# Optimization experiments

Hardware: AMD Instinct MI355X
Metric: run time of the kernel (lower is better)

## Reference

```python
import jax, jax.numpy as jnp
import numpy as np

N_NODES = 100000
N_EDGES = 1250000
IN_DIM = 64
HID_DIM = 64
EDGE_DIM = 10
BN_EPS = 1e-5


def setup_inputs() -> dict:
    key = jax.random.key(0)
    ks = jax.random.split(key, 10)
    x = jax.random.normal(ks[0], (N_NODES, IN_DIM), dtype=jnp.float32)
    edge_index = jax.random.randint(ks[1], (2, N_EDGES), 0, N_NODES, dtype=jnp.int64)
    edge_attr = jax.random.normal(ks[2], (N_EDGES, EDGE_DIM), dtype=jnp.float32)
    # GINEConv edge projection Linear(edge_dim=10 -> indim)
    W_edge = jax.random.normal(ks[3], (EDGE_DIM, IN_DIM), dtype=jnp.float32) * (1.0 / np.sqrt(EDGE_DIM))
    b_edge = jnp.zeros((IN_DIM,), dtype=jnp.float32)
    # MLP: Linear(indim, hiddendim) -> ReLU -> Linear(hiddendim, hiddendim)
    W1 = jax.random.normal(ks[4], (IN_DIM, HID_DIM), dtype=jnp.float32) * (1.0 / np.sqrt(IN_DIM))
    b1 = jnp.zeros((HID_DIM,), dtype=jnp.float32)
    W2 = jax.random.normal(ks[5], (HID_DIM, HID_DIM), dtype=jnp.float32) * (1.0 / np.sqrt(HID_DIM))
    b2 = jnp.zeros((HID_DIM,), dtype=jnp.float32)
    # BatchNorm1d affine params
    bn_gamma = jnp.ones((HID_DIM,), dtype=jnp.float32)
    bn_beta = jnp.zeros((HID_DIM,), dtype=jnp.float32)
    return {"x": x, "edge_index": edge_index, "edge_attr": edge_attr,
            "W_edge": W_edge, "b_edge": b_edge, "W1": W1, "b1": b1,
            "W2": W2, "b2": b2, "bn_gamma": bn_gamma, "bn_beta": bn_beta}


def reference(x, edge_index, edge_attr, W_edge, b_edge, W1, b1, W2, b2, bn_gamma, bn_beta):
    src, dst = edge_index[0], edge_index[1]
    # message: ReLU(x_j + lin(edge_attr))  [E, indim]
    msg = jax.nn.relu(x[src] + edge_attr @ W_edge + b_edge)
    # sum-aggregate into destination nodes  [N, indim]
    aggr = jax.ops.segment_sum(msg, dst, num_segments=N_NODES)
    # GIN update: nn((1+eps)*x + aggr), eps=0
    h = x + aggr
    h = jax.nn.relu(h @ W1 + b1) @ W2 + b2
    # outer ReLU then BatchNorm1d (training-mode batch stats)
    h = jax.nn.relu(h)
    mean = jnp.mean(h, axis=0)
    var = jnp.var(h, axis=0)
    out = (h - mean) * jax.lax.rsqrt(var + BN_EPS) * bn_gamma + bn_beta
    return out
```

## Files before the change

kernel.cpp:

```cpp
#include <hip/hip_runtime.h>

#define N_NODES 100000
#define N_EDGES 1250000
#define DIM 64
#define EDGE_DIM 10
#define BN_EPS 1e-5f

#define SCAN_CHUNK 1024
#define NB_SCAN ((N_NODES + SCAN_CHUNK - 1) / SCAN_CHUNK)

#define DEG_OFF    0
#define SUMS_OFF_I (DEG_OFF + N_NODES)
#define OFFS_OFF   (SUMS_OFF_I + 256)
#define CUR_OFF    (OFFS_OFF + N_NODES)
#define BSUM_OFF   (CUR_OFF + N_NODES)
#define REC_OFF    (BSUM_OFF + 128)

__device__ __forceinline__ unsigned f2bf(float f) {
    unsigned b = __float_as_uint(f);
    return (b + 0x7FFFu + ((b >> 16) & 1u)) >> 16;
}

extern "C" __global__ __launch_bounds__(256)
void prep_kernel(const float* __restrict__ x, unsigned short* __restrict__ xh,
                 const int* __restrict__ ei, int* __restrict__ deg)
{
    int t = blockIdx.x * 256 + threadIdx.x;
    int stride = gridDim.x * 256;
    for (int i = t; i < N_NODES * DIM / 4; i += stride) {
        float4 v = ((const float4*)x)[i];
        uint2 p;
        p.x = f2bf(v.x) | (f2bf(v.y) << 16);
        p.y = f2bf(v.z) | (f2bf(v.w) << 16);
        ((uint2*)xh)[i] = p;
    }
    for (int e = t; e < N_EDGES; e += stride) {
        unsigned d = (unsigned)ei[N_EDGES + e];
        d = d < N_NODES ? d : (N_NODES - 1);
        atomicAdd(&deg[d], 1);
    }
}

extern "C" __global__ __launch_bounds__(256)
void scan_bsum_kernel(const int* __restrict__ deg, int* __restrict__ bsum)
{
    __shared__ int sw[4];
    int tid = threadIdx.x;
    int base = blockIdx.x * SCAN_CHUNK + tid * 4;
    int s = 0;
    #pragma unroll
    for (int j = 0; j < 4; ++j) {
        int idx = base + j;
        if (idx < N_NODES) s += deg[idx];
    }
    #pragma unroll
    for (int m = 1; m < 64; m <<= 1) s += __shfl_xor(s, m, 64);
    if ((tid & 63) == 0) sw[tid >> 6] = s;
    __syncthreads();
    if (tid == 0) bsum[blockIdx.x] = sw[0] + sw[1] + sw[2] + sw[3];
}

extern "C" __global__ __launch_bounds__(128)
void scan_top_kernel(int* __restrict__ bsum)
{
    __shared__ int s[128];
    int tid = threadIdx.x;
    int v = (tid < NB_SCAN) ? bsum[tid] : 0;
    s[tid] = v;
    __syncthreads();
    #pragma unroll
    for (int off = 1; off < 128; off <<= 1) {
        int t = (tid >= off) ? s[tid - off] : 0;
        __syncthreads();
        s[tid] += t;
        __syncthreads();
    }
    if (tid < NB_SCAN) bsum[tid] = s[tid] - v;
}

extern "C" __global__ __launch_bounds__(256)
void scan_final_kernel(const int* __restrict__ deg, const int* __restrict__ bsum,
                       int* __restrict__ offs, int* __restrict__ cur)
{
    __shared__ int s[256];
    int tid = threadIdx.x;
    int base = blockIdx.x * SCAN_CHUNK + tid * 4;
    int d[4];
    #pragma unroll
    for (int j = 0; j < 4; ++j) {
        int idx = base + j;
        d[j] = (idx < N_NODES) ? deg[idx] : 0;
    }
    int tot = d[0] + d[1] + d[2] + d[3];
    s[tid] = tot;
    __syncthreads();
    #pragma unroll
    for (int off = 1; off < 256; off <<= 1) {
        int t = (tid >= off) ? s[tid - off] : 0;
        __syncthreads();
        s[tid] += t;
        __syncthreads();
    }
    int b = bsum[blockIdx.x] + s[tid] - tot;
    #pragma unroll
    for (int j = 0; j < 4; ++j) {
        int idx = base + j;
        if (idx < N_NODES) { offs[idx] = b; cur[idx] = b; }
        b += d[j];
    }
}

extern "C" __global__ __launch_bounds__(256)
void scatter_kernel(const int* __restrict__ ei, const float* __restrict__ ea,
                    int* __restrict__ cur, int* __restrict__ recs, int fast)
{
    int e = blockIdx.x * 256 + threadIdx.x;
    if (e >= N_EDGES) return;
    unsigned d = (unsigned)ei[N_EDGES + e];
    unsigned s = (unsigned)ei[e];
    d = d < N_NODES ? d : (N_NODES - 1);
    s = s < N_NODES ? s : (N_NODES - 1);
    int pos = atomicAdd(&cur[d], 1);
    if (fast) {
        const float* a = ea + (size_t)e * EDGE_DIM;
        unsigned w[5];
        #pragma unroll
        for (int k = 0; k < 5; ++k) {
            float2 p = *(const float2*)&a[2 * k];
            w[k] = f2bf(p.x) | (f2bf(p.y) << 16);
        }
        int2* r = (int2*)(recs + (size_t)pos * 6);
        r[0] = make_int2((int)s, (int)w[0]);
        r[1] = make_int2((int)w[1], (int)w[2]);
        r[2] = make_int2((int)w[3], (int)w[4]);
    } else {
        ((int2*)recs)[pos] = make_int2((int)s, e);
    }
}


#define SLOT_ACC(W0, Bv, Cv, Xv, MK)                                            \
    {                                                                           \
        float m0 = bias4.x, m1 = bias4.y, m2 = bias4.z, m3 = bias4.w;           \
        unsigned wd_; float a_;                                                 \
        wd_ = (unsigned)(W0);                                                   \
        a_ = __uint_as_float(wd_ << 16);                                        \
        m0 = fmaf(a_, wc[0].x, m0); m1 = fmaf(a_, wc[0].y, m1);                 \
        m2 = fmaf(a_, wc[0].z, m2); m3 = fmaf(a_, wc[0].w, m3);                 \
        a_ = __uint_as_float(wd_ & 0xFFFF0000u);                                \
        m0 = fmaf(a_, wc[1].x, m0); m1 = fmaf(a_, wc[1].y, m1);                 \
        m2 = fmaf(a_, wc[1].z, m2); m3 = fmaf(a_, wc[1].w, m3);                 \
        wd_ = (unsigned)(Bv).x;                                                 \
        a_ = __uint_as_float(wd_ << 16);                                        \
        m0 = fmaf(a_, wc[2].x, m0); m1 = fmaf(a_, wc[2].y, m1);                 \
        m2 = fmaf(a_, wc[2].z, m2); m3 = fmaf(a_, wc[2].w, m3);                 \
        a_ = __uint_as_float(wd_ & 0xFFFF0000u);                                \
        m0 = fmaf(a_, wc[3].x, m0); m1 = fmaf(a_, wc[3].y, m1);                 \
        m2 = fmaf(a_, wc[3].z, m2); m3 = fmaf(a_, wc[3].w, m3);                 \
        wd_ = (unsigned)(Bv).y;                                                 \
        a_ = __uint_as_float(wd_ << 16);                                        \
        m0 = fmaf(a_, wc[4].x, m0); m1 = fmaf(a_, wc[4].y, m1);                 \
        m2 = fmaf(a_, wc[4].z, m2); m3 = fmaf(a_, wc[4].w, m3);                 \
        a_ = __uint_as_float(wd_ & 0xFFFF0000u);                                \
        m0 = fmaf(a_, wc[5].x, m0); m1 = fmaf(a_, wc[5].y, m1);                 \
        m2 = fmaf(a_, wc[5].z, m2); m3 = fmaf(a_, wc[5].w, m3);                 \
        wd_ = (unsigned)(Cv).x;                                                 \
        a_ = __uint_as_float(wd_ << 16);                                        \
        m0 = fmaf(a_, wc[6].x, m0); m1 = fmaf(a_, wc[6].y, m1);                 \
        m2 = fmaf(a_, wc[6].z, m2); m3 = fmaf(a_, wc[6].w, m3);                 \
        a_ = __uint_as_float(wd_ & 0xFFFF0000u);                                \
        m0 = fmaf(a_, wc[7].x, m0); m1 = fmaf(a_, wc[7].y, m1);                 \
        m2 = fmaf(a_, wc[7].z, m2); m3 = fmaf(a_, wc[7].w, m3);                 \
        wd_ = (unsigned)(Cv).y;                                                 \
        a_ = __uint_as_float(wd_ << 16);                                        \
        m0 = fmaf(a_, wc[8].x, m0); m1 = fmaf(a_, wc[8].y, m1);                 \
        m2 = fmaf(a_, wc[8].z, m2); m3 = fmaf(a_, wc[8].w, m3);                 \
        a_ = __uint_as_float(wd_ & 0xFFFF0000u);                                \
        m0 = fmaf(a_, wc[9].x, m0); m1 = fmaf(a_, wc[9].y, m1);                 \
        m2 = fmaf(a_, wc[9].z, m2); m3 = fmaf(a_, wc[9].w, m3);                 \
        float x0_ = __uint_as_float(((unsigned)(Xv).x) << 16);                  \
        float x1_ = __uint_as_float(((unsigned)(Xv).x) & 0xFFFF0000u);          \
        float x2_ = __uint_as_float(((unsigned)(Xv).y) << 16);                  \
        float x3_ = __uint_as_float(((unsigned)(Xv).y) & 0xFFFF0000u);          \
        float c0_ = fmaxf(m0 + x0_, 0.0f);                                      \
        float c1_ = fmaxf(m1 + x1_, 0.0f);                                      \
        float c2_ = fmaxf(m2 + x2_, 0.0f);                                      \
        float c3_ = fmaxf(m3 + x3_, 0.0f);                                      \
        ax += (MK) ? c0_ : 0.0f; ay += (MK) ? c1_ : 0.0f;                       \
        az += (MK) ? c2_ : 0.0f; aw += (MK) ? c3_ : 0.0f;                       \
    }

extern "C" __global__ __launch_bounds__(512)
void node_csr_kernel(const unsigned short* __restrict__ xh,
                     const float* __restrict__ ea,
                     const float* __restrict__ We,
                     const float* __restrict__ be,
                     const int* __restrict__ offs,
                     const int* __restrict__ cur,
                     const int* __restrict__ recs,
                     const float* __restrict__ W1,
                     const float* __restrict__ b1,
                     const float* __restrict__ W2,
                     const float* __restrict__ b2,
                     float* __restrict__ out,
                     float* __restrict__ sums,
                     int fast)
{
    __shared__ __align__(16) float sW[DIM * DIM];
    __shared__ __align__(16) float sT[DIM * 68];
    __shared__ int sOffs[64];
    __shared__ int sCur[64];

    int tid  = threadIdx.x;
    int lane = tid & 63;
    int wv   = tid >> 6;
    int base = blockIdx.x * 64;

    int fq = lane & 15;
    int q  = lane >> 4;

    for (int i = tid; i < DIM * DIM; i += 512) sW[i] = W1[i];
    if (tid < 64) {
        int v = base + tid;
        v = v < N_NODES ? v : (N_NODES - 1);
        sOffs[tid] = offs[v];
    } else if (tid < 128) {
        int v = base + tid - 64;
        v = v < N_NODES ? v : (N_NODES - 1);
        sCur[tid - 64] = cur[v];
    }

    float4 wc[EDGE_DIM];
    #pragma unroll
    for (int k = 0; k < EDGE_DIM; ++k)
        wc[k] = *(const float4*)&We[k * DIM + 4 * fq];
    float4 bias4 = *(const float4*)&be[4 * fq];

    const uint2* xq2 = (const uint2*)xh;
    const int2*  rc2 = (const int2*)recs;

    __syncthreads();

    if (fast) {
        int2 A0, A1, A2, A3;
        bool haveA = false;
        #pragma unroll 1
        for (int t = 0; t < 8; ++t) {
            int nl = wv * 8 + t;
            int v  = base + nl;
            float ax = 0.f, ay = 0.f, az = 0.f, aw = 0.f;
            unsigned vc = (unsigned)(v < N_NODES ? v : (N_NODES - 1));
            uint2 sx = xq2[vc * 16u + (unsigned)fq];
            if (v < N_NODES) {
                int stt = __builtin_amdgcn_readfirstlane(sOffs[nl]);
                int end = __builtin_amdgcn_readfirstlane(sCur[nl]);
                int ng  = (end - stt + 15) >> 4;
                #pragma unroll 1
                for (int g = 0; g < ng; ++g) {
                    int i0e = stt + g * 16;
                    int e1  = end - 1;
                    int s0 = i0e + q, s1 = s0 + 4, s2 = s0 + 8, s3 = s0 + 12;
                    int c0 = 3 * min(s0, e1), c1 = 3 * min(s1, e1);
                    int c2 = 3 * min(s2, e1), c3 = 3 * min(s3, e1);
                    if (!haveA) {
                        A0 = rc2[c0]; A1 = rc2[c1]; A2 = rc2[c2]; A3 = rc2[c3];
                    }
                    int2 B0 = rc2[c0 + 1], C0 = rc2[c0 + 2];
                    int2 B1 = rc2[c1 + 1], C1 = rc2[c1 + 2];
                    int2 B2 = rc2[c2 + 1], C2 = rc2[c2 + 2];
                    int2 B3 = rc2[c3 + 1], C3 = rc2[c3 + 2];
                    unsigned u0 = (unsigned)A0.x; u0 = u0 < N_NODES ? u0 : 0u;
                    unsigned u1 = (unsigned)A1.x; u1 = u1 < N_NODES ? u1 : 0u;
                    unsigned u2 = (unsigned)A2.x; u2 = u2 < N_NODES ? u2 : 0u;
                    unsigned u3 = (unsigned)A3.x; u3 = u3 < N_NODES ? u3 : 0u;
                    uint2 X0 = xq2[u0 * 16u + (unsigned)fq];
                    uint2 X1 = xq2[u1 * 16u + (unsigned)fq];
                    uint2 X2 = xq2[u2 * 16u + (unsigned)fq];
                    uint2 X3 = xq2[u3 * 16u + (unsigned)fq];
                    unsigned w00 = (unsigned)A0.y, w01 = (unsigned)A1.y;
                    unsigned w02 = (unsigned)A2.y, w03 = (unsigned)A3.y;
                    haveA = false;
                    {
                        int tn = t, gn = g + 1, sttn = stt, endn = end;
                        bool ok = (gn < ng);
                        if (!ok) {
                            tn = t + 1; gn = 0;
                            if (tn < 8) {
                                int nln = wv * 8 + tn;
                                int vn  = base + nln;
                                if (vn < N_NODES) {
                                    sttn = __builtin_amdgcn_readfirstlane(sOffs[nln]);
                                    endn = __builtin_amdgcn_readfirstlane(sCur[nln]);
                                    ok = endn > sttn;
                                }
                            }
                        }
                        if (ok) {
                            int i0n = sttn + gn * 16;
                            int en1 = endn - 1;
                            int n0 = 3 * min(i0n + q,      en1);
                            int n1 = 3 * min(i0n + q + 4,  en1);
                            int n2 = 3 * min(i0n + q + 8,  en1);
                            int n3 = 3 * min(i0n + q + 12, en1);
                            A0 = rc2[n0]; A1 = rc2[n1]; A2 = rc2[n2]; A3 = rc2[n3];
                            haveA = true;
                        }
                    }
                    SLOT_ACC(w00, B0, C0, X0, s0 < end);
                    SLOT_ACC(w01, B1, C1, X1, s1 < end);
                    SLOT_ACC(w02, B2, C2, X2, s2 < end);
                    SLOT_ACC(w03, B3, C3, X3, s3 < end);
                }
            }
            ax += __shfl_xor(ax, 16, 64); ax += __shfl_xor(ax, 32, 64);
            ay += __shfl_xor(ay, 16, 64); ay += __shfl_xor(ay, 32, 64);
            az += __shfl_xor(az, 16, 64); az += __shfl_xor(az, 32, 64);
            aw += __shfl_xor(aw, 16, 64); aw += __shfl_xor(aw, 32, 64);
            if (v < N_NODES) {
                ax += __uint_as_float(sx.x << 16);
                ay += __uint_as_float(sx.x & 0xFFFF0000u);
                az += __uint_as_float(sx.y << 16);
                aw += __uint_as_float(sx.y & 0xFFFF0000u);
            }
            if (q == 0) {
                sT[(4 * fq + 0) * 68 + nl] = ax;
                sT[(4 * fq + 1) * 68 + nl] = ay;
                sT[(4 * fq + 2) * 68 + nl] = az;
                sT[(4 * fq + 3) * 68 + nl] = aw;
            }
        }
    } else {
        #pragma unroll 1
        for (int t = 0; t < 8; ++t) {
            int nl = wv * 8 + t;
            int v  = base + nl;
            float ax = 0.f, ay = 0.f, az = 0.f, aw = 0.f;
            unsigned vc = (unsigned)(v < N_NODES ? v : (N_NODES - 1));
            uint2 sx = xq2[vc * 16u + (unsigned)fq];
            if (v < N_NODES) {
                int stt = __builtin_amdgcn_readfirstlane(sOffs[nl]);
                int end = __builtin_amdgcn_readfirstlane(sCur[nl]);
                int ng  = (end - stt + 15) >> 4;
                #pragma unroll 1
                for (int g = 0; g < ng; ++g) {
                    int i0e = stt + g * 16;
                    int e1  = end - 1;
                    int s0 = i0e + q, s1 = s0 + 4, s2 = s0 + 8, s3 = s0 + 12;
                    int2 A0 = ((const int2*)recs)[min(s0, e1)];
                    int2 A1 = ((const int2*)recs)[min(s1, e1)];
                    int2 A2 = ((const int2*)recs)[min(s2, e1)];
                    int2 A3 = ((const int2*)recs)[min(s3, e1)];
                    unsigned u0 = (unsigned)A0.x; u0 = u0 < N_NODES ? u0 : 0u;
                    unsigned u1 = (unsigned)A1.x; u1 = u1 < N_NODES ? u1 : 0u;
                    unsigned u2 = (unsigned)A2.x; u2 = u2 < N_NODES ? u2 : 0u;
                    unsigned u3 = (unsigned)A3.x; u3 = u3 < N_NODES ? u3 : 0u;
                    uint2 X0 = xq2[u0 * 16u + (unsigned)fq];
                    uint2 X1 = xq2[u1 * 16u + (unsigned)fq];
                    uint2 X2 = xq2[u2 * 16u + (unsigned)fq];
                    uint2 X3 = xq2[u3 * 16u + (unsigned)fq];
                    #pragma unroll
                    for (int p = 0; p < 4; ++p) {
                        int sl = p == 0 ? s0 : p == 1 ? s1 : p == 2 ? s2 : s3;
                        unsigned ue = (unsigned)(p == 0 ? A0.y : p == 1 ? A1.y :
                                                 p == 2 ? A2.y : A3.y);
                        ue = ue < N_EDGES ? ue : 0u;
                        uint2 Xv = p == 0 ? X0 : p == 1 ? X1 : p == 2 ? X2 : X3;
                        const float* a = ea + (size_t)ue * EDGE_DIM;
                        float m0 = bias4.x, m1 = bias4.y, m2 = bias4.z, m3 = bias4.w;
                        #pragma unroll
                        for (int k = 0; k < EDGE_DIM; ++k) {
                            float av = a[k];
                            m0 = fmaf(av, wc[k].x, m0);
                            m1 = fmaf(av, wc[k].y, m1);
                            m2 = fmaf(av, wc[k].z, m2);
                            m3 = fmaf(av, wc[k].w, m3);
                        }
                        float x0_ = __uint_as_float(Xv.x << 16);
                        float x1_ = __uint_as_float(Xv.x & 0xFFFF0000u);
                        float x2_ = __uint_as_float(Xv.y << 16);
                        float x3_ = __uint_as_float(Xv.y & 0xFFFF0000u);
                        bool mk = sl < end;
                        ax += mk ? fmaxf(m0 + x0_, 0.f) : 0.f;
                        ay += mk ? fmaxf(m1 + x1_, 0.f) : 0.f;
                        az += mk ? fmaxf(m2 + x2_, 0.f) : 0.f;
                        aw += mk ? fmaxf(m3 + x3_, 0.f) : 0.f;
                    }
                }
            }
            ax += __shfl_xor(ax, 16, 64); ax += __shfl_xor(ax, 32, 64);
            ay += __shfl_xor(ay, 16, 64); ay += __shfl_xor(ay, 32, 64);
            az += __shfl_xor(az, 16, 64); az += __shfl_xor(az, 32, 64);
            aw += __shfl_xor(aw, 16, 64); aw += __shfl_xor(aw, 32, 64);
            if (v < N_NODES) {
                ax += __uint_as_float(sx.x << 16);
                ay += __uint_as_float(sx.x & 0xFFFF0000u);
                az += __uint_as_float(sx.y << 16);
                aw += __uint_as_float(sx.y & 0xFFFF0000u);
            }
            if (q == 0) {
                sT[(4 * fq + 0) * 68 + nl] = ax;
                sT[(4 * fq + 1) * 68 + nl] = ay;
                sT[(4 * fq + 2) * 68 + nl] = az;
                sT[(4 * fq + 3) * 68 + nl] = aw;
            }
        }
    }
    __syncthreads();

    int i0 = (tid & 15) * 4;
    int j0 = (tid >> 4) * 2;

    float acc1g[4][2] = {};
    #pragma unroll 8
    for (int k = 0; k < DIM; ++k) {
        float4 av = *(const float4*)&sT[k * 68 + i0];
        float bw0 = sW[k * DIM + j0];
        float bw1 = sW[k * DIM + j0 + 1];
        float a4[4] = {av.x, av.y, av.z, av.w};
        #pragma unroll
        for (int a = 0; a < 4; ++a) {
            acc1g[a][0] = fmaf(a4[a], bw0, acc1g[a][0]);
            acc1g[a][1] = fmaf(a4[a], bw1, acc1g[a][1]);
        }
    }
    __syncthreads();

    for (int i = tid; i < DIM * DIM; i += 512) sW[i] = W2[i];

    float b1a[2] = {b1[j0], b1[j0 + 1]};
    float tv[4][2];
    #pragma unroll
    for (int a = 0; a < 4; ++a)
        #pragma unroll
        for (int b = 0; b < 2; ++b)
            tv[a][b] = fmaxf(acc1g[a][b] + b1a[b], 0.0f);

    #pragma unroll
    for (int b = 0; b < 2; ++b) {
        float4 w = make_float4(tv[0][b], tv[1][b], tv[2][b], tv[3][b]);
        *(float4*)&sT[(j0 + b) * 68 + i0] = w;
    }
    __syncthreads();

    float acc2[4][2] = {};
    #pragma unroll 8
    for (int k = 0; k < DIM; ++k) {
        float4 av = *(const float4*)&sT[k * 68 + i0];
        float bw0 = sW[k * DIM + j0];
        float bw1 = sW[k * DIM + j0 + 1];
        float a4[4] = {av.x, av.y, av.z, av.w};
        #pragma unroll
        for (int a = 0; a < 4; ++a) {
            acc2[a][0] = fmaf(a4[a], bw0, acc2[a][0]);
            acc2[a][1] = fmaf(a4[a], bw1, acc2[a][1]);
        }
    }

    float b2a[2] = {b2[j0], b2[j0 + 1]};
    float ps[2] = {0.f, 0.f};
    float pq[2] = {0.f, 0.f};
    #pragma unroll
    for (int a = 0; a < 4; ++a) {
        int n = base + i0 + a;
        float r0 = fmaxf(acc2[a][0] + b2a[0], 0.0f);
        float r1 = fmaxf(acc2[a][1] + b2a[1], 0.0f);
        if (n < N_NODES) {
            float2 w = make_float2(r0, r1);
            *(float2*)&out[(size_t)n * DIM + j0] = w;
            ps[0] += r0; ps[1] += r1;
            pq[0] += r0 * r0; pq[1] += r1 * r1;
        }
    }

    #pragma unroll
    for (int m = 1; m < 16; m <<= 1) {
        #pragma unroll
        for (int b = 0; b < 2; ++b) {
            ps[b] += __shfl_xor(ps[b], m, 64);
            pq[b] += __shfl_xor(pq[b], m, 64);
        }
    }
    if ((lane & 15) == 0) {
        #pragma unroll
        for (int b = 0; b < 2; ++b) {
            unsafeAtomicAdd(&sums[j0 + b], ps[b]);
            unsafeAtomicAdd(&sums[64 + j0 + b], pq[b]);
        }
    }
}

extern "C" __global__ __launch_bounds__(256)
void bn_apply_kernel(float* __restrict__ out, const float* __restrict__ sums,
                     const float* __restrict__ gamma, const float* __restrict__ beta)
{
    int j = blockIdx.x * 256 + threadIdx.x;
    int f0 = (j & 15) * 4;
    float4 s1 = *(const float4*)&sums[f0];
    float4 s2 = *(const float4*)&sums[64 + f0];
    float4 gm = *(const float4*)&gamma[f0];
    float4 bt = *(const float4*)&beta[f0];
    const float inv_n = 1.0f / (float)N_NODES;
    float4 sc, sh;
    {
        float m = s1.x * inv_n; float vv = fmaf(-m, m, s2.x * inv_n);
        sc.x = gm.x * rsqrtf(vv + BN_EPS); sh.x = fmaf(-m, sc.x, bt.x);
    }
    {
        float m = s1.y * inv_n; float vv = fmaf(-m, m, s2.y * inv_n);
        sc.y = gm.y * rsqrtf(vv + BN_EPS); sh.y = fmaf(-m, sc.y, bt.y);
    }
    {
        float m = s1.z * inv_n; float vv = fmaf(-m, m, s2.z * inv_n);
        sc.z = gm.z * rsqrtf(vv + BN_EPS); sh.z = fmaf(-m, sc.z, bt.z);
    }
    {
        float m = s1.w * inv_n; float vv = fmaf(-m, m, s2.w * inv_n);
        sc.w = gm.w * rsqrtf(vv + BN_EPS); sh.w = fmaf(-m, sc.w, bt.w);
    }
    float4 v = ((float4*)out)[j];
    v.x = fmaf(v.x, sc.x, sh.x);
    v.y = fmaf(v.y, sc.y, sh.y);
    v.z = fmaf(v.z, sc.z, sh.z);
    v.w = fmaf(v.w, sc.w, sh.w);
    ((float4*)out)[j] = v;
}

extern "C" void kernel_launch(void* const* d_in, const int* in_sizes, int n_in,
                              void* d_out, int out_size, void* d_ws, size_t ws_size,
                              hipStream_t stream)
{
    const float* x     = (const float*)d_in[0];
    const int*   ei    = (const int*)  d_in[1];
    const float* ea    = (const float*)d_in[2];
    const float* We    = (const float*)d_in[3];
    const float* be    = (const float*)d_in[4];
    const float* W1    = (const float*)d_in[5];
    const float* b1    = (const float*)d_in[6];
    const float* W2    = (const float*)d_in[7];
    const float* b2    = (const float*)d_in[8];
    const float* gamma = (const float*)d_in[9];
    const float* beta  = (const float*)d_in[10];

    float* out  = (float*)d_out;
    int*   wsi  = (int*)d_ws;
    int*   deg  = wsi + DEG_OFF;
    float* sums = (float*)(wsi + SUMS_OFF_I);
    int*   offs = wsi + OFFS_OFF;
    int*   cur  = wsi + CUR_OFF;
    int*   bsum = wsi + BSUM_OFF;
    int*   recs = wsi + REC_OFF;

    size_t need_fast = ((size_t)REC_OFF + 6u * N_EDGES + (size_t)N_NODES * DIM / 2) * 4u;
    int fast = (ws_size >= need_fast) ? 1 : 0;
    int rec_ints = fast ? 6 * N_EDGES : 2 * N_EDGES;
    unsigned short* xh = (unsigned short*)(wsi + REC_OFF + rec_ints);

    hipMemsetAsync(wsi, 0, (size_t)(N_NODES + 256) * sizeof(int), stream);

    prep_kernel<<<2048, 256, 0, stream>>>(x, xh, ei, deg);
    scan_bsum_kernel<<<NB_SCAN, 256, 0, stream>>>(deg, bsum);
    scan_top_kernel<<<1, 128, 0, stream>>>(bsum);
    scan_final_kernel<<<NB_SCAN, 256, 0, stream>>>(deg, bsum, offs, cur);
    scatter_kernel<<<(N_EDGES + 255) / 256, 256, 0, stream>>>(ei, ea, cur, recs, fast);

    node_csr_kernel<<<(N_NODES + 63) / 64, 512, 0, stream>>>(
        xh, ea, We, be, offs, cur, recs, W1, b1, W2, b2, out, sums, fast);

    bn_apply_kernel<<<(N_NODES * DIM / 4) / 256, 256, 0, stream>>>(out, sums, gamma, beta);
}
```

Baseline: 449.2 us.

## Split fused CSR aggregation and MLP into separate aggr and mlp kernels

The fused node kernel, which gathered neighbor messages and then ran the two-layer MLP in shared memory, is split into two kernels. The new aggr_kernel handles 8 nodes per 256-thread block and writes the aggregated features to global memory, reusing the output buffer. A separate mlp_kernel reads those features back, transposes them into shared memory and runs the MLP and BN statistics. The aim is finer-grained load balancing and higher occupancy for the irregular gather. The cost is an extra global round trip of N×64 floats and one more launch, and the software prefetch of the next record group is dropped.

Result: slower. 492.7 us (+9.7%).

```diff
diff --git a/kernel.cpp b/kernel.cpp
--- a/kernel.cpp
+++ b/kernel.cpp
@@ -137,7 +137,6 @@
         ((int2*)recs)[pos] = make_int2((int)s, e);
     }
 }
-
 
 #define SLOT_ACC(W0, Bv, Cv, Xv, MK)                                            \
     {                                                                           \
@@ -190,45 +189,22 @@
         az += (MK) ? c2_ : 0.0f; aw += (MK) ? c3_ : 0.0f;                       \
     }
 
-extern "C" __global__ __launch_bounds__(512)
-void node_csr_kernel(const unsigned short* __restrict__ xh,
-                     const float* __restrict__ ea,
-                     const float* __restrict__ We,
-                     const float* __restrict__ be,
-                     const int* __restrict__ offs,
-                     const int* __restrict__ cur,
-                     const int* __restrict__ recs,
-                     const float* __restrict__ W1,
-                     const float* __restrict__ b1,
-                     const float* __restrict__ W2,
-                     const float* __restrict__ b2,
-                     float* __restrict__ out,
-                     float* __restrict__ sums,
-                     int fast)
-{
-    __shared__ __align__(16) float sW[DIM * DIM];
-    __shared__ __align__(16) float sT[DIM * 68];
-    __shared__ int sOffs[64];
-    __shared__ int sCur[64];
-
+extern "C" __global__ __launch_bounds__(256)
+void aggr_kernel(const unsigned short* __restrict__ xh,
+                 const float* __restrict__ ea,
+                 const float* __restrict__ We,
+                 const float* __restrict__ be,
+                 const int* __restrict__ offs,
+                 const int* __restrict__ cur,
+                 const int* __restrict__ recs,
+                 float* __restrict__ aggr,
+                 int fast)
+{
     int tid  = threadIdx.x;
     int lane = tid & 63;
     int wv   = tid >> 6;
-    int base = blockIdx.x * 64;
-
-    int fq = lane & 15;
-    int q  = lane >> 4;
-
-    for (int i = tid; i < DIM * DIM; i += 512) sW[i] = W1[i];
-    if (tid < 64) {
-        int v = base + tid;
-        v = v < N_NODES ? v : (N_NODES - 1);
-        sOffs[tid] = offs[v];
-    } else if (tid < 128) {
-        int v = base + tid - 64;
-        v = v < N_NODES ? v : (N_NODES - 1);
-        sCur[tid - 64] = cur[v];
-    }
+    int fq   = lane & 15;
+    int q    = lane >> 4;
 
     float4 wc[EDGE_DIM];
     #pragma unroll
@@ -239,171 +215,135 @@
     const uint2* xq2 = (const uint2*)xh;
     const int2*  rc2 = (const int2*)recs;
 
-    __syncthreads();
-
-    if (fast) {
-        int2 A0, A1, A2, A3;
-        bool haveA = false;
-        #pragma unroll 1
-        for (int t = 0; t < 8; ++t) {
-            int nl = wv * 8 + t;
-            int v  = base + nl;
-            float ax = 0.f, ay = 0.f, az = 0.f, aw = 0.f;
-            unsigned vc = (unsigned)(v < N_NODES ? v : (N_NODES - 1));
-            uint2 sx = xq2[vc * 16u + (unsigned)fq];
-            if (v < N_NODES) {
-                int stt = __builtin_amdgcn_readfirstlane(sOffs[nl]);
-                int end = __builtin_amdgcn_readfirstlane(sCur[nl]);
-                int ng  = (end - stt + 15) >> 4;
-                #pragma unroll 1
-                for (int g = 0; g < ng; ++g) {
-                    int i0e = stt + g * 16;
-                    int e1  = end - 1;
-                    int s0 = i0e + q, s1 = s0 + 4, s2 = s0 + 8, s3 = s0 + 12;
-                    int c0 = 3 * min(s0, e1), c1 = 3 * min(s1, e1);
-                    int c2 = 3 * min(s2, e1), c3 = 3 * min(s3, e1);
-                    if (!haveA) {
-                        A0 = rc2[c0]; A1 = rc2[c1]; A2 = rc2[c2]; A3 = rc2[c3];
+    #pragma unroll 1
+    for (int t = 0; t < 2; ++t) {
+        int v = blockIdx.x * 8 + wv * 2 + t;
+        if (v >= N_NODES) break;
+        uint2 sx = xq2[(unsigned)v * 16u + (unsigned)fq];
+        int stt = __builtin_amdgcn_readfirstlane(offs[v]);
+        int end = __builtin_amdgcn_readfirstlane(cur[v]);
+        float ax = 0.f, ay = 0.f, az = 0.f, aw = 0.f;
+        int ng = (end - stt + 15) >> 4;
+        if (fast) {
+            #pragma unroll 1
+            for (int g = 0; g < ng; ++g) {
+                int i0e = stt + g * 16;
+                int e1  = end - 1;
+                int s0 = i0e + q, s1 = s0 + 4, s2 = s0 + 8, s3 = s0 + 12;
+                int c0 = 3 * min(s0, e1), c1 = 3 * min(s1, e1);
+                int c2 = 3 * min(s2, e1), c3 = 3 * min(s3, e1);
+                int2 A0 = rc2[c0],     A1 = rc2[c1];
+                int2 A2 = rc2[c2],     A3 = rc2[c3];
+                int2 B0 = rc2[c0 + 1], C0 = rc2[c0 + 2];
+                int2 B1 = rc2[c1 + 1], C1 = rc2[c1 + 2];
+                int2 B2 = rc2[c2 + 1], C2 = rc2[c2 + 2];
+                int2 B3 = rc2[c3 + 1], C3 = rc2[c3 + 2];
+                unsigned u0 = (unsigned)A0.x; u0 = u0 < N_NODES ? u0 : 0u;
+                unsigned u1 = (unsigned)A1.x; u1 = u1 < N_NODES ? u1 : 0u;
+                unsigned u2 = (unsigned)A2.x; u2 = u2 < N_NODES ? u2 : 0u;
+                unsigned u3 = (unsigned)A3.x; u3 = u3 < N_NODES ? u3 : 0u;
+                uint2 X0 = xq2[u0 * 16u + (unsigned)fq];
+                uint2 X1 = xq2[u1 * 16u + (unsigned)fq];
+                uint2 X2 = xq2[u2 * 16u + (unsigned)fq];
+                uint2 X3 = xq2[u3 * 16u + (unsigned)fq];
+                SLOT_ACC(A0.y, B0, C0, X0, s0 < end);
+                SLOT_ACC(A1.y, B1, C1, X1, s1 < end);
+                SLOT_ACC(A2.y, B2, C2, X2, s2 < end);
+                SLOT_ACC(A3.y, B3, C3, X3, s3 < end);
+            }
+        } else {
+            #pragma unroll 1
+            for (int g = 0; g < ng; ++g) {
+                int i0e = stt + g * 16;
+                int e1  = end - 1;
+                int s0 = i0e + q, s1 = s0 + 4, s2 = s0 + 8, s3 = s0 + 12;
+                int2 A0 = ((const int2*)recs)[min(s0, e1)];
+                int2 A1 = ((const int2*)recs)[min(s1, e1)];
+                int2 A2 = ((const int2*)recs)[min(s2, e1)];
+                int2 A3 = ((const int2*)recs)[min(s3, e1)];
+                unsigned u0 = (unsigned)A0.x; u0 = u0 < N_NODES ? u0 : 0u;
+                unsigned u1 = (unsigned)A1.x; u1 = u1 < N_NODES ? u1 : 0u;
+                unsigned u2 = (unsigned)A2.x; u2 = u2 < N_NODES ? u2 : 0u;
+                unsigned u3 = (unsigned)A3.x; u3 = u3 < N_NODES ? u3 : 0u;
+                uint2 X0 = xq2[u0 * 16u + (unsigned)fq];
+                uint2 X1 = xq2[u1 * 16u + (unsigned)fq];
+                uint2 X2 = xq2[u2 * 16u + (unsigned)fq];
+                uint2 X3 = xq2[u3 * 16u + (unsigned)fq];
+                #pragma unroll
+                for (int p = 0; p < 4; ++p) {
+                    int sl = p == 0 ? s0 : p == 1 ? s1 : p == 2 ? s2 : s3;
+                    unsigned ue = (unsigned)(p == 0 ? A0.y : p == 1 ? A1.y :
+                                             p == 2 ? A2.y : A3.y);
+                    ue = ue < N_EDGES ? ue : 0u;
+                    uint2 Xv = p == 0 ? X0 : p == 1 ? X1 : p == 2 ? X2 : X3;
+                    const float* a = ea + (size_t)ue * EDGE_DIM;
+                    float m0 = bias4.x, m1 = bias4.y, m2 = bias4.z, m3 = bias4.w;
+                    #pragma unroll
+                    for (int k = 0; k < EDGE_DIM; ++k) {
+                        float av = a[k];
+                        m0 = fmaf(av, wc[k].x, m0);
+                        m1 = fmaf(av, wc[k].y, m1);
+                        m2 = fmaf(av, wc[k].z, m2);
+                        m3 = fmaf(av, wc[k].w, m3);
                     }
-                    int2 B0 = rc2[c0 + 1], C0 = rc2[c0 + 2];
-                    int2 B1 = rc2[c1 + 1], C1 = rc2[c1 + 2];
-                    int2 B2 = rc2[c2 + 1], C2 = rc2[c2 + 2];
-                    int2 B3 = rc2[c3 + 1], C3 = rc2[c3 + 2];
-                    unsigned u0 = (unsigned)A0.x; u0 = u0 < N_NODES ? u0 : 0u;
-                    unsigned u1 = (unsigned)A1.x; u1 = u1 < N_NODES ? u1 : 0u;
-                    unsigned u2 = (unsigned)A2.x; u2 = u2 < N_NODES ? u2 : 0u;
-                    unsigned u3 = (unsigned)A3.x; u3 = u3 < N_NODES ? u3 : 0u;
-                    uint2 X0 = xq2[u0 * 16u + (unsigned)fq];
-                    uint2 X1 = xq2[u1 * 16u + (unsigned)fq];
-                    uint2 X2 = xq2[u2 * 16u + (unsigned)fq];
-                    uint2 X3 = xq2[u3 * 16u + (unsigned)fq];
-                    unsigned w00 = (unsigned)A0.y, w01 = (unsigned)A1.y;
-                    unsigned w02 = (unsigned)A2.y, w03 = (unsigned)A3.y;
-                    haveA = false;
-                    {
-                        int tn = t, gn = g + 1, sttn = stt, endn = end;
-                        bool ok = (gn < ng);
-                        if (!ok) {
-                            tn = t + 1; gn = 0;
-                            if (tn < 8) {
-                                int nln = wv * 8 + tn;
-                                int vn  = base + nln;
-                                if (vn < N_NODES) {
-                                    sttn = __builtin_amdgcn_readfirstlane(sOffs[nln]);
-                                    endn = __builtin_amdgcn_readfirstlane(sCur[nln]);
-                                    ok = endn > sttn;
-                                }
-                            }
-                        }
-                        if (ok) {
-                            int i0n = sttn + gn * 16;
-                            int en1 = endn - 1;
-                            int n0 = 3 * min(i0n + q,      en1);
-                            int n1 = 3 * min(i0n + q + 4,  en1);
-                            int n2 = 3 * min(i0n + q + 8,  en1);
-                            int n3 = 3 * min(i0n + q + 12, en1);
-                            A0 = rc2[n0]; A1 = rc2[n1]; A2 = rc2[n2]; A3 = rc2[n3];
-                            haveA = true;
-                        }
-                    }
-                    SLOT_ACC(w00, B0, C0, X0, s0 < end);
-                    SLOT_ACC(w01, B1, C1, X1, s1 < end);
-                    SLOT_ACC(w02, B2, C2, X2, s2 < end);
-                    SLOT_ACC(w03, B3, C3, X3, s3 < end);
+                    float x0_ = __uint_as_float(Xv.x << 16);
+                    float x1_ = __uint_as_float(Xv.x & 0xFFFF0000u);
+                    float x2_ = __uint_as_float(Xv.y << 16);
+                    float x3_ = __uint_as_float(Xv.y & 0xFFFF0000u);
+                    bool mk = sl < end;
+                    ax += mk ? fmaxf(m0 + x0_, 0.f) : 0.f;
+                    ay += mk ? fmaxf(m1 + x1_, 0.f) : 0.f;
+                    az += mk ? fmaxf(m2 + x2_, 0.f) : 0.f;
+                    aw += mk ? fmaxf(m3 + x3_, 0.f) : 0.f;
                 }
             }
-            ax += __shfl_xor(ax, 16, 64); ax += __shfl_xor(ax, 32, 64);
-            ay += __shfl_xor(ay, 16, 64); ay += __shfl_xor(ay, 32, 64);
-            az += __shfl_xor(az, 16, 64); az += __shfl_xor(az, 32, 64);
-            aw += __shfl_xor(aw, 16, 64); aw += __shfl_xor(aw, 32, 64);
-            if (v < N_NODES) {
-                ax += __uint_as_float(sx.x << 16);
-                ay += __uint_as_float(sx.x & 0xFFFF0000u);
-                az += __uint_as_float(sx.y << 16);
-                aw += __uint_as_float(sx.y & 0xFFFF0000u);
-            }
-            if (q == 0) {
-                sT[(4 * fq + 0) * 68 + nl] = ax;
-                sT[(4 * fq + 1) * 68 + nl] = ay;
-                sT[(4 * fq + 2) * 68 + nl] = az;
-                sT[(4 * fq + 3) * 68 + nl] = aw;
-            }
-        }
-    } else {
-        #pragma unroll 1
-        for (int t = 0; t < 8; ++t) {
-            int nl = wv * 8 + t;
-            int v  = base + nl;
-            float ax = 0.f, ay = 0.f, az = 0.f, aw = 0.f;
-            unsigned vc = (unsigned)(v < N_NODES ? v : (N_NODES - 1));
-            uint2 sx = xq2[vc * 16u + (unsigned)fq];
-            if (v < N_NODES) {
-                int stt = __builtin_amdgcn_readfirstlane(sOffs[nl]);
-                int end = __builtin_amdgcn_readfirstlane(sCur[nl]);
-                int ng  = (end - stt + 15) >> 4;
-                #pragma unroll 1
-                for (int g = 0; g < ng; ++g) {
-                    int i0e = stt + g * 16;
-                    int e1  = end - 1;
-                    int s0 = i0e + q, s1 = s0 + 4, s2 = s0 + 8, s3 = s0 + 12;
-                    int2 A0 = ((const int2*)recs)[min(s0, e1)];
-                    int2 A1 = ((const int2*)recs)[min(s1, e1)];
-                    int2 A2 = ((const int2*)recs)[min(s2, e1)];
-                    int2 A3 = ((const int2*)recs)[min(s3, e1)];
-                    unsigned u0 = (unsigned)A0.x; u0 = u0 < N_NODES ? u0 : 0u;
-                    unsigned u1 = (unsigned)A1.x; u1 = u1 < N_NODES ? u1 : 0u;
-                    unsigned u2 = (unsigned)A2.x; u2 = u2 < N_NODES ? u2 : 0u;
-                    unsigned u3 = (unsigned)A3.x; u3 = u3 < N_NODES ? u3 : 0u;
-                    uint2 X0 = xq2[u0 * 16u + (unsigned)fq];
-                    uint2 X1 = xq2[u1 * 16u + (unsigned)fq];
-                    uint2 X2 = xq2[u2 * 16u + (unsigned)fq];
-                    uint2 X3 = xq2[u3 * 16u + (unsigned)fq];
-                    #pragma unroll
-                    for (int p = 0; p < 4; ++p) {
-                        int sl = p == 0 ? s0 : p == 1 ? s1 : p == 2 ? s2 : s3;
-                        unsigned ue = (unsigned)(p == 0 ? A0.y : p == 1 ? A1.y :
-                                                 p == 2 ? A2.y : A3.y);
-                        ue = ue < N_EDGES ? ue : 0u;
-                        uint2 Xv = p == 0 ? X0 : p == 1 ? X1 : p == 2 ? X2 : X3;
-                        const float* a = ea + (size_t)ue * EDGE_DIM;
-                        float m0 = bias4.x, m1 = bias4.y, m2 = bias4.z, m3 = bias4.w;
-                        #pragma unroll
-                        for (int k = 0; k < EDGE_DIM; ++k) {
-                            float av = a[k];
-                            m0 = fmaf(av, wc[k].x, m0);
-                            m1 = fmaf(av, wc[k].y, m1);
-                            m2 = fmaf(av, wc[k].z, m2);
-                            m3 = fmaf(av, wc[k].w, m3);
-                        }
-                        float x0_ = __uint_as_float(Xv.x << 16);
-                        float x1_ = __uint_as_float(Xv.x & 0xFFFF0000u);
-                        float x2_ = __uint_as_float(Xv.y << 16);
-                        float x3_ = __uint_as_float(Xv.y & 0xFFFF0000u);
-                        bool mk = sl < end;
-                        ax += mk ? fmaxf(m0 + x0_, 0.f) : 0.f;
-                        ay += mk ? fmaxf(m1 + x1_, 0.f) : 0.f;
-                        az += mk ? fmaxf(m2 + x2_, 0.f) : 0.f;
-                        aw += mk ? fmaxf(m3 + x3_, 0.f) : 0.f;
-                    }
-                }
-            }
-            ax += __shfl_xor(ax, 16, 64); ax += __shfl_xor(ax, 32, 64);
-            ay += __shfl_xor(ay, 16, 64); ay += __shfl_xor(ay, 32, 64);
-            az += __shfl_xor(az, 16, 64); az += __shfl_xor(az, 32, 64);
-            aw += __shfl_xor(aw, 16, 64); aw += __shfl_xor(aw, 32, 64);
-            if (v < N_NODES) {
-                ax += __uint_as_float(sx.x << 16);
-                ay += __uint_as_float(sx.x & 0xFFFF0000u);
-                az += __uint_as_float(sx.y << 16);
-                aw += __uint_as_float(sx.y & 0xFFFF0000u);
-            }
-            if (q == 0) {
-                sT[(4 * fq + 0) * 68 + nl] = ax;
-                sT[(4 * fq + 1) * 68 + nl] = ay;
-                sT[(4 * fq + 2) * 68 + nl] = az;
-                sT[(4 * fq + 3) * 68 + nl] = aw;
-            }
-        }
+        }
+        ax += __shfl_xor(ax, 16, 64); ax += __shfl_xor(ax, 32, 64);
+        ay += __shfl_xor(ay, 16, 64); ay += __shfl_xor(ay, 32, 64);
+        az += __shfl_xor(az, 16, 64); az += __shfl_xor(az, 32, 64);
+        aw += __shfl_xor(aw, 16, 64); aw += __shfl_xor(aw, 32, 64);
+        ax += __uint_as_float(sx.x << 16);
+        ay += __uint_as_float(sx.x & 0xFFFF0000u);
+        az += __uint_as_float(sx.y << 16);
+        aw += __uint_as_float(sx.y & 0xFFFF0000u);
+        if (q == 0)
+            *(float4*)&aggr[(size_t)v * DIM + 4 * fq] =
+                make_float4(ax, ay, az, aw);
+    }
+}
+
+extern "C" __global__ __launch_bounds__(512)
+void mlp_kernel(const float* __restrict__ W1,
+                const float* __restrict__ b1,
+                const float* __restrict__ W2,
+                const float* __restrict__ b2,
+                float* __restrict__ out,
+                float* __restrict__ sums)
+{
+    __shared__ __align__(16) float sW[DIM * DIM];
+    __shared__ __align__(16) float sT[DIM * 68];
+
+    int tid  = threadIdx.x;
+    int lane = tid & 63;
+    int base = blockIdx.x * 64;
+
+    for (int i = tid; i < DIM * DIM; i += 512) sW[i] = W1[i];
+
+    {
+        int nl = tid >> 3;
+        int fo = (tid & 7) * 8;
+        int v  = base + nl;
+        v = v < N_NODES ? v : (N_NODES - 1);
+        const float4* row = (const float4*)&out[(size_t)v * DIM + fo];
+        float4 a0 = row[0], a1 = row[1];
+        sT[(fo + 0) * 68 + nl] = a0.x;
+        sT[(fo + 1) * 68 + nl] = a0.y;
+        sT[(fo + 2) * 68 + nl] = a0.z;
+        sT[(fo + 3) * 68 + nl] = a0.w;
+        sT[(fo + 4) * 68 + nl] = a1.x;
+        sT[(fo + 5) * 68 + nl] = a1.y;
+        sT[(fo + 6) * 68 + nl] = a1.z;
+        sT[(fo + 7) * 68 + nl] = a1.w;
     }
     __syncthreads();
 
@@ -563,8 +503,11 @@
     scan_final_kernel<<<NB_SCAN, 256, 0, stream>>>(deg, bsum, offs, cur);
     scatter_kernel<<<(N_EDGES + 255) / 256, 256, 0, stream>>>(ei, ea, cur, recs, fast);
 
-    node_csr_kernel<<<(N_NODES + 63) / 64, 512, 0, stream>>>(
-        xh, ea, We, be, offs, cur, recs, W1, b1, W2, b2, out, sums, fast);
+    aggr_kernel<<<(N_NODES + 7) / 8, 256, 0, stream>>>(
+        xh, ea, We, be, offs, cur, recs, out, fast);
+
+    mlp_kernel<<<(N_NODES + 63) / 64, 512, 0, stream>>>(
+        W1, b1, W2, b2, out, sums);
 
     bn_apply_kernel<<<(N_NODES * DIM / 4) / 256, 256, 0, stream>>>(out, sums, gamma, beta);
 }
```
